# Kernel optimization log

Measured on AMD Instinct MI355X. Metric: run time of the kernel, lower is better.

## Reference

```python
import jax, jax.numpy as jnp
import numpy as np
import math

N_EMBD = 768
N_HEAD = 12
B, T = 4, 1024


def setup_inputs() -> dict:
    key = jax.random.key(0)
    ks = jax.random.split(key, 12)
    s = 0.02
    d = N_EMBD
    inp = {
        'x': jax.random.normal(ks[0], (B, T, d), dtype=jnp.float32),
        'refractory_state': jax.random.uniform(ks[1], (B, T), dtype=jnp.float32),
        'ln1_w': jnp.ones((d,), jnp.float32),
        'ln1_b': jnp.zeros((d,), jnp.float32),
        'c_attn_w': jax.random.normal(ks[2], (d, 3 * d), dtype=jnp.float32) * s,
        'c_attn_b': jnp.zeros((3 * d,), jnp.float32),
        'c_proj_w': jax.random.normal(ks[3], (d, d), dtype=jnp.float32) * s,
        'c_proj_b': jnp.zeros((d,), jnp.float32),
        'threshold': jnp.full((N_HEAD,), 0.01, jnp.float32),
        'leak': jnp.full((N_HEAD,), 2.0, jnp.float32),
        'steepness': jnp.full((N_HEAD,), 2.0, jnp.float32),
        'refractory_strength': jnp.full((N_HEAD,), -2.0, jnp.float32),
        'cross_layer_weight': jnp.full((N_HEAD,), -2.0, jnp.float32),
        'ln2_w': jnp.ones((d,), jnp.float32),
        'ln2_b': jnp.zeros((d,), jnp.float32),
        'fc_w': jax.random.normal(ks[4], (d, 4 * d), dtype=jnp.float32) * s,
        'fc_b': jnp.zeros((4 * d,), jnp.float32),
        'proj_w': jax.random.normal(ks[5], (4 * d, d), dtype=jnp.float32) * s,
        'proj_b': jnp.zeros((d,), jnp.float32),
    }
    return inp


def _layer_norm(x, w, b, eps=1e-5):
    m = jnp.mean(x, axis=-1, keepdims=True)
    v = jnp.var(x, axis=-1, keepdims=True)
    return (x - m) * jax.lax.rsqrt(v + eps) * w + b


def _per_head(p):
    # [H] -> [1, H, 1, 1]
    return p.reshape(1, -1, 1, 1)


def ember_block(x, refractory_state, ln1_w, ln1_b, c_attn_w, c_attn_b,
                c_proj_w, c_proj_b, threshold, leak, steepness,
                refractory_strength, cross_layer_weight,
                ln2_w, ln2_b, fc_w, fc_b, proj_w, proj_b):
    Bx, Tx, C = x.shape
    hd = C // N_HEAD

    h = _layer_norm(x, ln1_w, ln1_b)
    qkv = h @ c_attn_w + c_attn_b
    q, k, v = jnp.split(qkv, 3, axis=-1)
    # [B, T, C] -> [B, H, T, hd]
    q = q.reshape(Bx, Tx, N_HEAD, hd).transpose(0, 2, 1, 3)
    k = k.reshape(Bx, Tx, N_HEAD, hd).transpose(0, 2, 1, 3)
    v = v.reshape(Bx, Tx, N_HEAD, hd).transpose(0, 2, 1, 3)

    att = jnp.einsum('bhqd,bhkd->bhqk', q, k) * (1.0 / math.sqrt(hd))
    causal = jnp.tril(jnp.ones((Tx, Tx), dtype=bool))
    att = jnp.where(causal, att, -jnp.inf)
    att_probs = jax.nn.softmax(att, axis=-1)

    # per-head LIF modulation with refractory dynamics
    thr = jnp.abs(_per_head(threshold)) * 0.1
    lk = jax.nn.sigmoid(_per_head(leak))
    stp = jax.nn.softplus(_per_head(steepness))

    column_load = att_probs.mean(axis=-2, keepdims=True)  # [B,H,1,T]
    ref_strength = jax.nn.softplus(_per_head(refractory_strength))
    eff_thr = thr + ref_strength * column_load
    cross_w = jax.nn.sigmoid(_per_head(cross_layer_weight))
    prev_load = refractory_state[:, None, None, :]  # [B,1,1,T]
    eff_thr = eff_thr + cross_w * prev_load

    fire_mask = jax.nn.sigmoid(stp * (att_probs - eff_thr))
    lif_weights = fire_mask + lk * (1.0 - fire_mask)
    modulated = att_probs * lif_weights
    modulated = modulated / (modulated.sum(axis=-1, keepdims=True) + 1e-8)
    new_refractory = modulated.mean(axis=1).mean(axis=-2)  # [B,T]

    y = jnp.einsum('bhqk,bhkd->bhqd', modulated, v)
    y = y.transpose(0, 2, 1, 3).reshape(Bx, Tx, C)
    y = y @ c_proj_w + c_proj_b
    x = x + y

    # MLP
    h2 = _layer_norm(x, ln2_w, ln2_b)
    h2 = jax.nn.gelu(h2 @ fc_w + fc_b, approximate=False)
    h2 = h2 @ proj_w + proj_b
    x = x + h2
    return x, new_refractory


def reference(x, refractory_state, ln1_w, ln1_b, c_attn_w, c_attn_b,
              c_proj_w, c_proj_b, threshold, leak, steepness,
              refractory_strength, cross_layer_weight,
              ln2_w, ln2_b, fc_w, fc_b, proj_w, proj_b):
    return ember_block(x, refractory_state, ln1_w, ln1_b, c_attn_w, c_attn_b,
                       c_proj_w, c_proj_b, threshold, leak, steepness,
                       refractory_strength, cross_layer_weight,
                       ln2_w, ln2_b, fc_w, fc_b, proj_w, proj_b)
```

## Files before the change

kernel.cpp:

```cpp
#include <hip/hip_runtime.h>
#include <hip/hip_bf16.h>
#include <math.h>

typedef unsigned short ushort;
typedef __attribute__((ext_vector_type(8))) unsigned short ushort8;
typedef __attribute__((ext_vector_type(8))) short s16x8;
typedef __attribute__((ext_vector_type(4))) float f32x4;

constexpr int NE = 768;
constexpr int NH = 12;
constexpr int HD = 64;
constexpr int Bc = 4;
constexpr int Tc = 1024;
constexpr int BT = Bc * Tc;

__device__ __forceinline__ ushort f2bf(float f) {
    __hip_bfloat16 h = __float2bfloat16(f);
    return *reinterpret_cast<ushort*>(&h);
}
__device__ __forceinline__ float bf2f(ushort u) {
    return __uint_as_float(((unsigned)u) << 16);
}
__device__ __forceinline__ float softplus_f(float x) {
    return (x > 20.f) ? x : log1pf(__expf(x));
}
__device__ __forceinline__ float rcp_f(float x) {
#if __has_builtin(__builtin_amdgcn_rcpf)
    return __builtin_amdgcn_rcpf(x);
#else
    return 1.f / x;
#endif
}
__device__ __forceinline__ void gload16(const void* g, void* l) {
    __builtin_amdgcn_global_load_lds((const __attribute__((address_space(1))) void*)g,
                                     (__attribute__((address_space(3))) void*)l, 16, 0, 0);
}

__global__ __launch_bounds__(256) void ln_kernel(const float* __restrict__ x,
                                                 const float* __restrict__ w,
                                                 const float* __restrict__ b,
                                                 ushort* __restrict__ out) {
    int row = blockIdx.x;
    const float* xr = x + (size_t)row * NE;
    int t = threadIdx.x;
    float v0 = xr[t], v1 = xr[t + 256], v2 = xr[t + 512];
    __shared__ float red[256], red2[256];
    red[t] = v0 + v1 + v2;
    red2[t] = v0 * v0 + v1 * v1 + v2 * v2;
    __syncthreads();
    for (int o = 128; o > 0; o >>= 1) {
        if (t < o) { red[t] += red[t + o]; red2[t] += red2[t + o]; }
        __syncthreads();
    }
    float mean = red[0] * (1.0f / NE);
    float var = red2[0] * (1.0f / NE) - mean * mean;
    float rs = rsqrtf(var + 1e-5f);
    ushort* orow = out + (size_t)row * NE;
    orow[t]       = f2bf((v0 - mean) * rs * w[t]       + b[t]);
    orow[t + 256] = f2bf((v1 - mean) * rs * w[t + 256] + b[t + 256]);
    orow[t + 512] = f2bf((v2 - mean) * rs * w[t + 512] + b[t + 512]);
}

__global__ __launch_bounds__(256) void wconvert(const float* __restrict__ W,
                                                ushort* __restrict__ Wt, int K, int N) {
    __shared__ float t[32][33];
    int n0 = blockIdx.x * 32, k0 = blockIdx.y * 32;
    int c = threadIdx.x & 31, r4 = threadIdx.x >> 5;
#pragma unroll
    for (int i = 0; i < 4; ++i) {
        int r = r4 + i * 8;
        t[r][c] = W[(size_t)(k0 + r) * N + n0 + c];
    }
    __syncthreads();
#pragma unroll
    for (int i = 0; i < 4; ++i) {
        int r = r4 + i * 8;
        Wt[(size_t)(n0 + r) * K + k0 + c] = f2bf(t[c][r]);
    }
}

template <int BM, int BN, int OUT_MODE, int ACT, bool RES>
__global__ __launch_bounds__(256) void mfma_gemm(
    const ushort* __restrict__ A, const ushort* __restrict__ Bt,
    const float* __restrict__ bias, const float* __restrict__ residual,
    float* __restrict__ Cf, ushort* __restrict__ Cb,
    ushort* __restrict__ Qo, ushort* __restrict__ Ko, ushort* __restrict__ Vo,
    int M, int N, int K, int NBX) {
    constexpr int NF = (BM == 128) ? 4 : 2;
    constexpr int MF = (BM == 64 && BN == 64) ? 2 : 4;
    constexpr int WN = BN / (NF * 16);
    constexpr int APASS = BM / 32, BPASS = BN / 32;
    __shared__ __align__(16) ushort As[BM * 64];
    __shared__ __align__(16) ushort Bs[BN * 64];
    int tid = threadIdx.x;
    int lane = tid & 63;
    int nb = gridDim.x;
    int lin = blockIdx.x;
    int nl = (lin & 7) * (nb >> 3) + (lin >> 3);
    int bx = nl % NBX, by = nl / NBX;
    int m0 = by * BM, n0 = bx * BN;
    int wave = tid >> 6;
    int wr = wave / WN, wc = wave % WN;
    f32x4 acc[MF][NF] = {};
    int srow = tid >> 3;
    int scol = (tid & 7) ^ (srow & 7);
    const ushort* ga = A + (size_t)(m0 + srow) * K + scol * 8;
    const ushort* gb = Bt + (size_t)(n0 + srow) * K + scol * 8;
    char* lA = (char*)As + tid * 16;
    char* lB = (char*)Bs + tid * 16;
    int fr = lane & 15, g = lane >> 4;
    unsigned swz = (unsigned)((fr & 7) << 4);
    const char* abase = (const char*)As + (wr * (MF * 16) + fr) * 128;
    const char* bbase = (const char*)Bs + (wc * (NF * 16) + fr) * 128;
    for (int k0 = 0; k0 < K; k0 += 64) {
#pragma unroll
        for (int p = 0; p < APASS; ++p)
            gload16(ga + (size_t)(p * 32) * K + k0, lA + p * 4096);
#pragma unroll
        for (int p = 0; p < BPASS; ++p)
            gload16(gb + (size_t)(p * 32) * K + k0, lB + p * 4096);
        __syncthreads();
#pragma unroll
        for (int ks = 0; ks < 2; ++ks) {
            unsigned o = ((unsigned)(g * 16 + ks * 64)) ^ swz;
            s16x8 af[MF], bf[NF];
#pragma unroll
            for (int i = 0; i < MF; ++i) af[i] = *(const s16x8*)(abase + i * 2048 + o);
#pragma unroll
            for (int i = 0; i < NF; ++i) bf[i] = *(const s16x8*)(bbase + i * 2048 + o);
#pragma unroll
            for (int mi = 0; mi < MF; ++mi)
#pragma unroll
                for (int ni = 0; ni < NF; ++ni)
                    acc[mi][ni] = __builtin_amdgcn_mfma_f32_16x16x32_bf16(af[mi], bf[ni], acc[mi][ni], 0, 0, 0);
        }
        __syncthreads();
    }
#pragma unroll
    for (int mi = 0; mi < MF; ++mi) {
#pragma unroll
        for (int ni = 0; ni < NF; ++ni) {
#pragma unroll
            for (int j = 0; j < 4; ++j) {
                int row = m0 + wr * (MF * 16) + mi * 16 + g * 4 + j;
                int col = n0 + wc * (NF * 16) + ni * 16 + fr;
                float v = acc[mi][ni][j] + bias[col];
                if (ACT == 1) v = 0.5f * v * (1.0f + erff(v * 0.70710678118654752f));
                if (RES) v += residual[(size_t)row * N + col];
                if (OUT_MODE == 0) {
                    Cf[(size_t)row * N + col] = v;
                } else if (OUT_MODE == 1) {
                    Cb[(size_t)row * N + col] = f2bf(v);
                } else {
                    int which = col >= 1536 ? 2 : (col >= 768 ? 1 : 0);
                    int rem = col - which * 768;
                    int hh = rem >> 6, d = rem & 63;
                    int b_ = row >> 10, t_ = row & 1023;
                    if (which == 2)
                        Vo[((size_t)(b_ * NH + hh) * HD + d) * Tc + t_] = f2bf(v);
                    else {
                        ushort* dst = which == 0 ? Qo : Ko;
                        dst[((size_t)(b_ * NH + hh) * Tc + t_) * HD + d] = f2bf(v);
                    }
                }
            }
        }
    }
}


__global__ __launch_bounds__(128) void attn_P(
    const ushort* __restrict__ Qp, const ushort* __restrict__ Kp,
    ushort* __restrict__ Pbuf, float* __restrict__ denom, float* __restrict__ colsum) {
    int beta = blockIdx.x;
    int tq = 63 - beta / 48;
    int bh = beta % 48;
    int tid = threadIdx.x;
    int kh = tid >> 6, lane = tid & 63, qlane = lane & 15, g = lane >> 4;
    __shared__ ushort plds[2][16][48];
    __shared__ float cs[1056];
    __shared__ float dden[2][16];
    int nst = (tq + 2) >> 1;
    int smid = (nst + 1) >> 1;
    int slo = kh ? smid : 0, shi = kh ? nst : smid;
    int kmaxc = (tq + 1) * 16;
    for (int i = tid; i < 1056; i += 128) cs[i] = 0.f;
    const ushort* Qb = Qp + (size_t)bh * Tc * HD;
    const ushort* Kb = Kp + (size_t)bh * Tc * HD;
    const ushort* qr = Qb + (size_t)(tq * 16 + qlane) * HD + g * 8;
    s16x8 qf0 = *(const s16x8*)qr;
    s16x8 qf1 = *(const s16x8*)(qr + 32);
    ushort* panel = Pbuf + ((size_t)bh * 1056 + (unsigned)(((tq + 1) * (tq + 1)) >> 2)) * 512;
    int q = tq * 16 + qlane;
    float dpart = 0.f;
    for (int s = slo; s < shi; ++s) {
        int kt0 = 2 * s, kt1 = 2 * s + 1;
        {
            const ushort* kr = Kb + (size_t)(kt0 * 16 + qlane) * HD + g * 8;
            s16x8 kf0 = *(const s16x8*)kr;
            s16x8 kf1 = *(const s16x8*)(kr + 32);
            f32x4 z = {0.f, 0.f, 0.f, 0.f};
            z = __builtin_amdgcn_mfma_f32_16x16x32_bf16(kf0, qf0, z, 0, 0, 0);
            z = __builtin_amdgcn_mfma_f32_16x16x32_bf16(kf1, qf1, z, 0, 0, 0);
#pragma unroll
            for (int j = 0; j < 4; ++j) {
                int key = kt0 * 16 + g * 4 + j;
                float p = (key <= q) ? __expf(z[j] * 0.125f - 8.f) : 0.f;
                dpart += p;
                plds[kh][qlane][g * 4 + j] = f2bf(p);
            }
        }
        if (kt1 <= tq) {
            const ushort* kr = Kb + (size_t)(kt1 * 16 + qlane) * HD + g * 8;
            s16x8 kf0 = *(const s16x8*)kr;
            s16x8 kf1 = *(const s16x8*)(kr + 32);
            f32x4 z = {0.f, 0.f, 0.f, 0.f};
            z = __builtin_amdgcn_mfma_f32_16x16x32_bf16(kf0, qf0, z, 0, 0, 0);
            z = __builtin_amdgcn_mfma_f32_16x16x32_bf16(kf1, qf1, z, 0, 0, 0);
#pragma unroll
            for (int j = 0; j < 4; ++j) {
                int key = kt1 * 16 + g * 4 + j;
                float p = (key <= q) ? __expf(z[j] * 0.125f - 8.f) : 0.f;
                dpart += p;
                plds[kh][qlane][16 + g * 4 + j] = f2bf(p);
            }
        } else {
#pragma unroll
            for (int j = 0; j < 4; ++j) plds[kh][qlane][16 + g * 4 + j] = 0;
        }
        s16x8 pa = *(const s16x8*)&plds[kh][qlane][g * 8];
        *(s16x8*)(panel + (size_t)s * 512 + lane * 8) = pa;
    }
    dpart += __shfl_xor(dpart, 16);
    dpart += __shfl_xor(dpart, 32);
    if (lane < 16) dden[kh][lane] = dpart;
    __syncthreads();
    float dsum = dden[0][qlane] + dden[1][qlane];
    if (tid < 16) denom[(size_t)bh * Tc + tq * 16 + tid] = dden[0][tid] + dden[1][tid];
    float dinvq = rcp_f(dsum);
    for (int s = slo; s < shi; ++s) {
        s16x8 v8 = *(const s16x8*)(panel + (size_t)s * 512 + lane * 8);
        int k0 = s * 32 + g * 8;
#pragma unroll
        for (int j = 0; j < 8; ++j) {
            float r = bf2f((ushort)v8[j]) * dinvq;
            r += __shfl_xor(r, 1);
            r += __shfl_xor(r, 2);
            r += __shfl_xor(r, 4);
            r += __shfl_xor(r, 8);
            if (qlane == 0) cs[k0 + j] += r;
        }
    }
    __syncthreads();
    for (int i = tid; i < kmaxc; i += 128)
        atomicAdd(&colsum[(size_t)bh * Tc + i], cs[i]);
}

__global__ __launch_bounds__(128) void attn_CD(
    const ushort* __restrict__ Pbuf, const ushort* __restrict__ Vt,
    const float* __restrict__ denom, const float* __restrict__ colsum,
    const float* __restrict__ refr_in,
    const float* __restrict__ threshold, const float* __restrict__ leak,
    const float* __restrict__ steepness, const float* __restrict__ refr_strength,
    const float* __restrict__ cross_w,
    ushort* __restrict__ ybuf, float* __restrict__ refr_out) {
    int beta = blockIdx.x;
    int tq = 63 - beta / 48;
    int bh = beta % 48;
    int b = bh / NH, h = bh - b * NH;
    int tid = threadIdx.x;
    int kh = tid >> 6, lane = tid & 63, qlane = lane & 15, g = lane >> 4;
    __shared__ float eff[1056];
    __shared__ float cs[1056];
    __shared__ float msum[2][16];
    __shared__ float minvL[16];
    __shared__ float ymrg[16][68];
    int nst = (tq + 2) >> 1;
    int smid = (nst + 1) >> 1;
    int slo = kh ? smid : 0, shi = kh ? nst : smid;
    int kmaxc = (tq + 1) * 16;
    float thr = fabsf(threshold[h]) * 0.1f;
    float lk = 1.f / (1.f + __expf(-leak[h]));
    float lk1m = 1.f - lk;
    float stp = softplus_f(steepness[h]);
    float rfs = softplus_f(refr_strength[h]);
    float crw = 1.f / (1.f + __expf(-cross_w[h]));
    for (int i = tid; i < 1056; i += 128) {
        eff[i] = (i < kmaxc)
                     ? thr + rfs * (colsum[(size_t)bh * Tc + i] * (1.f / 1024.f))
                           + crw * refr_in[(size_t)b * Tc + i]
                     : 0.f;
        cs[i] = 0.f;
    }
    float dinvq = rcp_f(denom[(size_t)bh * Tc + tq * 16 + qlane]);
    __syncthreads();
    const ushort* panel =
        Pbuf + ((size_t)bh * 1056 + (unsigned)(((tq + 1) * (tq + 1)) >> 2)) * 512;
    s16x8 ptreg[16];
    float msp = 0.f;
#pragma unroll
    for (int ss = 0; ss < 16; ++ss) {
        int s = slo + ss;
        if (s < shi) {
            s16x8 v8 = *(const s16x8*)(panel + (size_t)s * 512 + lane * 8);
            int k0 = s * 32 + g * 8;
            s16x8 pw;
#pragma unroll
            for (int j = 0; j < 8; ++j) {
                float p = bf2f((ushort)v8[j]) * dinvq;
                float fire = rcp_f(1.f + __expf(-stp * (p - eff[k0 + j])));
                float pt = p * (lk + lk1m * fire);
                msp += pt;
                pw[j] = (short)f2bf(pt);
            }
            ptreg[ss] = pw;
        }
    }
    msp += __shfl_xor(msp, 16);
    msp += __shfl_xor(msp, 32);
    if (lane < 16) msum[kh][lane] = msp;
    __syncthreads();
    if (tid < 16) minvL[tid] = rcp_f(msum[0][tid] + msum[1][tid] + 1e-8f);
    __syncthreads();
    float minvq = minvL[qlane];
    const ushort* Vh = Vt + (size_t)bh * HD * Tc;
    f32x4 accY[4] = {};
#pragma unroll
    for (int ss = 0; ss < 16; ++ss) {
        int s = slo + ss;
        if (s < shi) {
            s16x8 pa = ptreg[ss];
            int k0 = s * 32 + g * 8;
#pragma unroll
            for (int j = 0; j < 8; ++j) {
                float r = bf2f((ushort)pa[j]) * minvq;
                r += __shfl_xor(r, 1);
                r += __shfl_xor(r, 2);
                r += __shfl_xor(r, 4);
                r += __shfl_xor(r, 8);
                if (qlane == 0) cs[k0 + j] += r;
            }
#pragma unroll
            for (int dt = 0; dt < 4; ++dt) {
                const ushort* vp = Vh + (size_t)(dt * 16 + qlane) * Tc + s * 32 + g * 8;
                s16x8 vf = *(const s16x8*)vp;
                accY[dt] = __builtin_amdgcn_mfma_f32_16x16x32_bf16(pa, vf, accY[dt], 0, 0, 0);
            }
        }
    }
    if (kh == 1) {
#pragma unroll
        for (int dt = 0; dt < 4; ++dt)
#pragma unroll
            for (int j = 0; j < 4; ++j)
                ymrg[g * 4 + j][dt * 16 + qlane] = accY[dt][j];
    }
    __syncthreads();
    if (kh == 0) {
#pragma unroll
        for (int dt = 0; dt < 4; ++dt)
#pragma unroll
            for (int j = 0; j < 4; ++j) {
                float y = (accY[dt][j] + ymrg[g * 4 + j][dt * 16 + qlane]) * minvL[g * 4 + j];
                ybuf[(size_t)(b * Tc + tq * 16 + g * 4 + j) * NE + h * 64 + dt * 16 + qlane] =
                    f2bf(y);
            }
    }
    for (int i = tid; i < kmaxc; i += 128)
        atomicAdd(&refr_out[(size_t)b * Tc + i], cs[i] * (1.f / (NH * Tc)));
}

extern "C" void kernel_launch(void* const* d_in, const int* in_sizes, int n_in,
                              void* d_out, int out_size, void* d_ws, size_t ws_size,
                              hipStream_t stream) {
    const float* x        = (const float*)d_in[0];
    const float* refr     = (const float*)d_in[1];
    const float* ln1_w    = (const float*)d_in[2];
    const float* ln1_b    = (const float*)d_in[3];
    const float* c_attn_w = (const float*)d_in[4];
    const float* c_attn_b = (const float*)d_in[5];
    const float* c_proj_w = (const float*)d_in[6];
    const float* c_proj_b = (const float*)d_in[7];
    const float* threshold = (const float*)d_in[8];
    const float* leak      = (const float*)d_in[9];
    const float* steepness = (const float*)d_in[10];
    const float* refractory_strength = (const float*)d_in[11];
    const float* cross_layer_weight  = (const float*)d_in[12];
    const float* ln2_w    = (const float*)d_in[13];
    const float* ln2_b    = (const float*)d_in[14];
    const float* fc_w     = (const float*)d_in[15];
    const float* fc_b     = (const float*)d_in[16];
    const float* proj_w   = (const float*)d_in[17];
    const float* proj_b   = (const float*)d_in[18];

    char* ws = (char*)d_ws;
    ushort* hbuf   = (ushort*)(ws + 0);
    ushort* qb     = (ushort*)(ws + 6291456);
    ushort* kb     = (ushort*)(ws + 12582912);
    ushort* vtg    = (ushort*)(ws + 18874368);
    ushort* ybuf   = (ushort*)(ws + 25165824);
    ushort* fc_act = (ushort*)(ws + 6291456);
    float*  denomb = (float*)(ws + 31457280);
    float*  colsum = (float*)(ws + 31653888);
    ushort* wt_attn  = (ushort*)(ws + 31850496);
    ushort* wt_cproj = (ushort*)(ws + 35389440);
    ushort* wt_fc    = (ushort*)(ws + 36569088);
    ushort* wt_proj  = (ushort*)(ws + 41287680);
    ushort* Pbuf     = (ushort*)(ws + 46006272);

    float* xout = (float*)d_out;
    float* refr_out = xout + (size_t)BT * NE;

    hipMemsetAsync(colsum, 0, (size_t)Bc * NH * Tc * sizeof(float), stream);
    hipMemsetAsync(refr_out, 0, (size_t)Bc * Tc * sizeof(float), stream);

    wconvert<<<dim3(2304 / 32, 768 / 32), 256, 0, stream>>>(c_attn_w, wt_attn, 768, 2304);
    wconvert<<<dim3(768 / 32, 768 / 32), 256, 0, stream>>>(c_proj_w, wt_cproj, 768, 768);
    wconvert<<<dim3(3072 / 32, 768 / 32), 256, 0, stream>>>(fc_w, wt_fc, 768, 3072);
    wconvert<<<dim3(768 / 32, 3072 / 32), 256, 0, stream>>>(proj_w, wt_proj, 3072, 768);

    ln_kernel<<<BT, 256, 0, stream>>>(x, ln1_w, ln1_b, hbuf);

    mfma_gemm<64, 128, 2, 0, false><<<1152, 256, 0, stream>>>(
        hbuf, wt_attn, c_attn_b, nullptr, nullptr, nullptr, qb, kb, vtg,
        BT, 3 * NE, NE, 18);

    attn_P<<<48 * 64, 128, 0, stream>>>(qb, kb, Pbuf, denomb, colsum);
    attn_CD<<<48 * 64, 128, 0, stream>>>(
        Pbuf, vtg, denomb, colsum, refr, threshold, leak, steepness,
        refractory_strength, cross_layer_weight, ybuf, refr_out);

    mfma_gemm<64, 64, 0, 0, true><<<768, 256, 0, stream>>>(
        ybuf, wt_cproj, c_proj_b, x, xout, nullptr, nullptr, nullptr, nullptr,
        BT, NE, NE, 12);

    ln_kernel<<<BT, 256, 0, stream>>>(xout, ln2_w, ln2_b, hbuf);

    mfma_gemm<128, 128, 1, 1, false><<<768, 256, 0, stream>>>(
        hbuf, wt_fc, fc_b, nullptr, nullptr, fc_act, nullptr, nullptr, nullptr,
        BT, 4 * NE, NE, 24);

    mfma_gemm<64, 64, 0, 0, true><<<768, 256, 0, stream>>>(
        fc_act, wt_proj, proj_b, xout, xout, nullptr, nullptr, nullptr, nullptr,
        BT, NE, 4 * NE, 12);
}
```

Before: 256.7 us.

## Double-buffer LDS in 64x64 GEMM tiles and merge weight-conversion launches

For the 64x64 GEMM configuration (c_proj and likely the MLP down-projection), the tile loop now double-buffers shared memory. It prefetches the next K-slice with async global-to-LDS loads while computing the current one, using explicit vmcnt waits and raw barriers. Separately, the four weight-transpose and bf16-conversion launches are merged into one kernel that dispatches tiles by block index. This aims to hide global-load latency and cut launch overhead, at the cost of more LDS per block and reliance on hand-tuned waitcnt counts.

```diff
diff --git a/kernel.cpp b/kernel.cpp
--- a/kernel.cpp
+++ b/kernel.cpp
@@ -61,11 +61,12 @@
     orow[t + 512] = f2bf((v2 - mean) * rs * w[t + 512] + b[t + 512]);
 }
 
-__global__ __launch_bounds__(256) void wconvert(const float* __restrict__ W,
-                                                ushort* __restrict__ Wt, int K, int N) {
+__device__ __forceinline__ void wconv_tile(const float* __restrict__ W,
+                                           ushort* __restrict__ Wt,
+                                           int K, int N, int bx, int by, int tid) {
     __shared__ float t[32][33];
-    int n0 = blockIdx.x * 32, k0 = blockIdx.y * 32;
-    int c = threadIdx.x & 31, r4 = threadIdx.x >> 5;
+    int n0 = bx * 32, k0 = by * 32;
+    int c = tid & 31, r4 = tid >> 5;
 #pragma unroll
     for (int i = 0; i < 4; ++i) {
         int r = r4 + i * 8;
@@ -76,6 +77,26 @@
     for (int i = 0; i < 4; ++i) {
         int r = r4 + i * 8;
         Wt[(size_t)(n0 + r) * K + k0 + c] = f2bf(t[c][r]);
+    }
+}
+
+__global__ __launch_bounds__(256) void wconvert_all(
+    const float* __restrict__ Wa, ushort* __restrict__ Ta,
+    const float* __restrict__ Wc, ushort* __restrict__ Tcp,
+    const float* __restrict__ Wf, ushort* __restrict__ Tf,
+    const float* __restrict__ Wp, ushort* __restrict__ Tp) {
+    int blk = blockIdx.x, tid = threadIdx.x;
+    if (blk < 1728) {
+        wconv_tile(Wa, Ta, 768, 2304, blk % 72, blk / 72, tid);
+    } else if (blk < 2304) {
+        int i = blk - 1728;
+        wconv_tile(Wc, Tcp, 768, 768, i % 24, i / 24, tid);
+    } else if (blk < 4608) {
+        int i = blk - 2304;
+        wconv_tile(Wf, Tf, 768, 3072, i % 96, i / 96, tid);
+    } else {
+        int i = blk - 4608;
+        wconv_tile(Wp, Tp, 3072, 768, i % 24, i / 24, tid);
     }
 }
 
@@ -90,8 +111,10 @@
     constexpr int MF = (BM == 64 && BN == 64) ? 2 : 4;
     constexpr int WN = BN / (NF * 16);
     constexpr int APASS = BM / 32, BPASS = BN / 32;
-    __shared__ __align__(16) ushort As[BM * 64];
-    __shared__ __align__(16) ushort Bs[BN * 64];
+    constexpr bool DBUF = (BM == 64 && BN == 64);
+    constexpr int NBUF = DBUF ? 2 : 1;
+    __shared__ __align__(16) ushort As[NBUF * BM * 64];
+    __shared__ __align__(16) ushort Bs[NBUF * BN * 64];
     int tid = threadIdx.x;
     int lane = tid & 63;
     int nb = gridDim.x;
@@ -112,29 +135,74 @@
     unsigned swz = (unsigned)((fr & 7) << 4);
     const char* abase = (const char*)As + (wr * (MF * 16) + fr) * 128;
     const char* bbase = (const char*)Bs + (wc * (NF * 16) + fr) * 128;
-    for (int k0 = 0; k0 < K; k0 += 64) {
-#pragma unroll
-        for (int p = 0; p < APASS; ++p)
-            gload16(ga + (size_t)(p * 32) * K + k0, lA + p * 4096);
-#pragma unroll
-        for (int p = 0; p < BPASS; ++p)
-            gload16(gb + (size_t)(p * 32) * K + k0, lB + p * 4096);
-        __syncthreads();
-#pragma unroll
-        for (int ks = 0; ks < 2; ++ks) {
-            unsigned o = ((unsigned)(g * 16 + ks * 64)) ^ swz;
-            s16x8 af[MF], bf[NF];
-#pragma unroll
-            for (int i = 0; i < MF; ++i) af[i] = *(const s16x8*)(abase + i * 2048 + o);
-#pragma unroll
-            for (int i = 0; i < NF; ++i) bf[i] = *(const s16x8*)(bbase + i * 2048 + o);
-#pragma unroll
-            for (int mi = 0; mi < MF; ++mi)
-#pragma unroll
-                for (int ni = 0; ni < NF; ++ni)
-                    acc[mi][ni] = __builtin_amdgcn_mfma_f32_16x16x32_bf16(af[mi], bf[ni], acc[mi][ni], 0, 0, 0);
-        }
-        __syncthreads();
+
+    if constexpr (DBUF) {
+        constexpr int ABYTES = BM * 64 * 2, BBYTES = BN * 64 * 2;
+        int nk = K >> 6;
+#pragma unroll
+        for (int p = 0; p < APASS; ++p) gload16(ga + (size_t)(p * 32) * K, lA + p * 4096);
+#pragma unroll
+        for (int p = 0; p < BPASS; ++p) gload16(gb + (size_t)(p * 32) * K, lB + p * 4096);
+        for (int k = 0; k < nk; ++k) {
+            int cur = k & 1;
+            if (k + 1 < nk) {
+                int nxt = cur ^ 1;
+                int k0 = (k + 1) << 6;
+#pragma unroll
+                for (int p = 0; p < APASS; ++p)
+                    gload16(ga + (size_t)(p * 32) * K + k0, lA + nxt * ABYTES + p * 4096);
+#pragma unroll
+                for (int p = 0; p < BPASS; ++p)
+                    gload16(gb + (size_t)(p * 32) * K + k0, lB + nxt * BBYTES + p * 4096);
+                asm volatile("s_waitcnt vmcnt(4)" ::: "memory");
+            } else {
+                asm volatile("s_waitcnt vmcnt(0)" ::: "memory");
+            }
+            __builtin_amdgcn_s_barrier();
+#pragma unroll
+            for (int ks = 0; ks < 2; ++ks) {
+                unsigned o = ((unsigned)(g * 16 + ks * 64)) ^ swz;
+                s16x8 af[MF], bf[NF];
+#pragma unroll
+                for (int i = 0; i < MF; ++i)
+                    af[i] = *(const s16x8*)(abase + cur * ABYTES + i * 2048 + o);
+#pragma unroll
+                for (int i = 0; i < NF; ++i)
+                    bf[i] = *(const s16x8*)(bbase + cur * BBYTES + i * 2048 + o);
+#pragma unroll
+                for (int mi = 0; mi < MF; ++mi)
+#pragma unroll
+                    for (int ni = 0; ni < NF; ++ni)
+                        acc[mi][ni] = __builtin_amdgcn_mfma_f32_16x16x32_bf16(af[mi], bf[ni], acc[mi][ni], 0, 0, 0);
+            }
+            asm volatile("s_waitcnt lgkmcnt(0)" ::: "memory");
+            __builtin_amdgcn_s_barrier();
+        }
+    } else {
+        for (int k0 = 0; k0 < K; k0 += 64) {
+#pragma unroll
+            for (int p = 0; p < APASS; ++p)
+                gload16(ga + (size_t)(p * 32) * K + k0, lA + p * 4096);
+#pragma unroll
+            for (int p = 0; p < BPASS; ++p)
+                gload16(gb + (size_t)(p * 32) * K + k0, lB + p * 4096);
+            __syncthreads();
+#pragma unroll
+            for (int ks = 0; ks < 2; ++ks) {
+                unsigned o = ((unsigned)(g * 16 + ks * 64)) ^ swz;
+                s16x8 af[MF], bf[NF];
+#pragma unroll
+                for (int i = 0; i < MF; ++i) af[i] = *(const s16x8*)(abase + i * 2048 + o);
+#pragma unroll
+                for (int i = 0; i < NF; ++i) bf[i] = *(const s16x8*)(bbase + i * 2048 + o);
+#pragma unroll
+                for (int mi = 0; mi < MF; ++mi)
+#pragma unroll
+                    for (int ni = 0; ni < NF; ++ni)
+                        acc[mi][ni] = __builtin_amdgcn_mfma_f32_16x16x32_bf16(af[mi], bf[ni], acc[mi][ni], 0, 0, 0);
+            }
+            __syncthreads();
+        }
     }
 #pragma unroll
     for (int mi = 0; mi < MF; ++mi) {
@@ -414,10 +482,8 @@
     hipMemsetAsync(colsum, 0, (size_t)Bc * NH * Tc * sizeof(float), stream);
     hipMemsetAsync(refr_out, 0, (size_t)Bc * Tc * sizeof(float), stream);
 
-    wconvert<<<dim3(2304 / 32, 768 / 32), 256, 0, stream>>>(c_attn_w, wt_attn, 768, 2304);
-    wconvert<<<dim3(768 / 32, 768 / 32), 256, 0, stream>>>(c_proj_w, wt_cproj, 768, 768);
-    wconvert<<<dim3(3072 / 32, 768 / 32), 256, 0, stream>>>(fc_w, wt_fc, 768, 3072);
-    wconvert<<<dim3(768 / 32, 3072 / 32), 256, 0, stream>>>(proj_w, wt_proj, 3072, 768);
+    wconvert_all<<<6912, 256, 0, stream>>>(c_attn_w, wt_attn, c_proj_w, wt_cproj,
+                                           fc_w, wt_fc, proj_w, wt_proj);
 
     ln_kernel<<<BT, 256, 0, stream>>>(x, ln1_w, ln1_b, hbuf);
 
```

Measured after the change: 252.0 us. About the same (-1.8%).
